# Kernel tuning notes

Hardware: AMD Instinct MI355X
Metric: run time of the kernel (lower is better)

## Reference

```python
import jax, jax.numpy as jnp
import numpy as np
import math

N = 60000; B = 2; D = 128; NH = 8; HD = D // NH; DFF = 256
NBLK = 6; L = NBLK * 2
WIN = 12.0; TEMP = 10000.0
NY, NX = 400, 400
MT = (36, 144)      # max_tokens per drop level (drop_info)
CAP = (25, 100)     # filled tokens per window in synthetic data (~0.7 fill)
LVL_N = (24000, 36000)  # voxels per drop level (per shift)


def _nwin(n, cap):
    return -(-n // cap)


def _make_inds(n, lvl):
    j = np.arange(n)
    return (j // CAP[lvl]) * MT[lvl] + (j % CAP[lvl])


def setup_inputs():
    ks = jax.random.split(jax.random.key(0), 8)
    rng = np.random.default_rng(0)
    # unique BEV coords per batch element -> scatter has no collisions
    coors_list = []
    for b in range(B):
        flat = rng.choice(NY * NX, N // B, replace=False)
        coors_list.append(np.stack([np.full(N // B, b, np.int64), np.zeros(N // B, np.int64), flat // NX, flat % NX], 1))
    coors = jnp.asarray(np.concatenate(coors_list, 0), dtype=jnp.int32)
    vxs, indss = [], []
    for s in range(2):
        perm = rng.permutation(N)
        vxs += [np.sort(perm[:LVL_N[0]]), np.sort(perm[LVL_N[0]:])]
        indss += [_make_inds(LVL_N[0], 0), _make_inds(LVL_N[1], 1)]
    i32 = lambda a: jnp.asarray(a, jnp.int32)
    f = lambda k, shape: jax.random.normal(k, shape, dtype=jnp.float32) * 0.02
    return dict(
        voxel_feat=jax.random.normal(ks[0], (N, D), dtype=jnp.float32),
        coors=coors,
        ciw0=jax.random.randint(ks[1], (N, 2), 0, int(WIN)).astype(jnp.float32),
        ciw1=jax.random.randint(ks[2], (N, 2), 0, int(WIN)).astype(jnp.float32),
        vx00=i32(vxs[0]), inds00=i32(indss[0]), vx01=i32(vxs[1]), inds01=i32(indss[1]),
        vx10=i32(vxs[2]), inds10=i32(indss[2]), vx11=i32(vxs[3]), inds11=i32(indss[3]),
        in_proj_w=f(ks[3], (L, 3 * D, D)), in_proj_b=jnp.zeros((L, 3 * D), jnp.float32),
        out_w=f(ks[4], (L, D, D)), out_b=jnp.zeros((L, D), jnp.float32),
        lin1_w=f(ks[5], (L, DFF, D)), lin1_b=jnp.zeros((L, DFF), jnp.float32),
        lin2_w=f(ks[6], (L, D, DFF)), lin2_b=jnp.zeros((L, D), jnp.float32),
        ln1_g=jnp.ones((L, D), jnp.float32), ln1_b=jnp.zeros((L, D), jnp.float32),
        ln2_g=jnp.ones((L, D), jnp.float32), ln2_b=jnp.zeros((L, D), jnp.float32),
        conv_w=f(ks[7], (2, D, D, 3, 3)),
        bn_g=jnp.ones((2, D), jnp.float32), bn_b=jnp.zeros((2, D), jnp.float32),
        bn_m=jnp.zeros((2, D), jnp.float32), bn_v=jnp.ones((2, D), jnp.float32),
    )


def _pos_embed(ciw):
    # SSTv1.get_pos_embed: interleaved sin/cos over x and y window coords
    xy = ciw - WIN / 2.0
    pl = D // 2
    i = jnp.arange(pl, dtype=jnp.float32)
    inv = TEMP ** (2.0 * jnp.floor(i / 2.0) / pl)
    e = xy[:, :, None] / inv                      # [N, 2, pl]
    emb = jnp.stack([jnp.sin(e[..., ::2]), jnp.cos(e[..., 1::2])], -1).reshape(ciw.shape[0], 2, pl)
    return jnp.concatenate([emb[:, 0], emb[:, 1]], -1)  # [N, D]


def _ln(x, g, b):
    mu = jnp.mean(x, -1, keepdims=True)
    var = jnp.mean((x - mu) ** 2, -1, keepdims=True)
    return (x - mu) * jax.lax.rsqrt(var + 1e-5) * g + b


def _forward(voxel_feat, coors, ciws, vx, inds, fp):
    (ipw, ipb, ow, ob, l1w, l1b, l2w, l2b, g1, b1, g2, b2, cw, bg, bb, bm, bv) = fp
    pos = [_pos_embed(ciws[0]), _pos_embed(ciws[1])]
    feat = voxel_feat
    for blk in range(NBLK):
        for s in range(2):  # BasicShiftBlock: one encoder layer per shift
            li = blk * 2 + s
            attn_out = jnp.zeros_like(feat)
            for lvl in range(2):  # drop levels, each with its own padded window tensor
                v, ii = vx[(s, lvl)], inds[(s, lvl)]
                mt = MT[lvl]
                nw = _nwin(int(v.shape[0]), CAP[lvl])
                def to_win(x2d):  # flat2window: scatter voxels into [nw, mt, C]
                    return jnp.zeros((nw * mt, x2d.shape[-1]), x2d.dtype).at[ii].set(x2d[v]).reshape(nw, mt, -1)
                wf = to_win(feat)
                wp = to_win(pos[s])
                pad = jnp.ones((nw * mt,), bool).at[ii].set(False).reshape(nw, mt)  # True = padded slot
                qk_in = wf + wp
                q = (qk_in @ ipw[li, :D].T + ipb[li, :D]).reshape(nw, mt, NH, HD)
                k = (qk_in @ ipw[li, D:2 * D].T + ipb[li, D:2 * D]).reshape(nw, mt, NH, HD)
                val = (wf @ ipw[li, 2 * D:].T + ipb[li, 2 * D:]).reshape(nw, mt, NH, HD)
                sc = jnp.einsum('wqhd,wkhd->whqk', q, k) / math.sqrt(HD)
                sc = jnp.where(pad[:, None, None, :], -jnp.inf, sc)
                o = jnp.einsum('whqk,wkhd->wqhd', jax.nn.softmax(sc, -1), val).reshape(nw, mt, D)
                o = o @ ow[li].T + ob[li]
                # window2flat: gather valid slots back to flat voxel order
                attn_out = attn_out.at[v].set(o.reshape(nw * mt, D)[ii])
            feat = _ln(feat + attn_out, g1[li], b1[li])
            h = jax.nn.gelu(feat @ l1w[li].T + l1b[li], approximate=False)
            feat = _ln(feat + h @ l2w[li].T + l2b[li], g2[li], b2[li])
    # recover_bev: scatter voxels into dense BEV canvas [B, C, ny, nx]
    flat_idx = coors[:, 0] * (NY * NX) + coors[:, 2] * NX + coors[:, 3]
    canvas = jnp.zeros((B * NY * NX, D), feat.dtype).at[flat_idx].set(feat)
    bev = canvas.reshape(B, NY, NX, D).transpose(0, 3, 1, 2)
    for i in range(2):  # attached dilated convs + BN(eval) + ReLU
        bev = jax.lax.conv_general_dilated(bev, cw[i], (1, 1), [(2, 2), (2, 2)], rhs_dilation=(2, 2), dimension_numbers=('NCHW', 'OIHW', 'NCHW'))
        bev = (bev - bm[i][:, None, None]) * jax.lax.rsqrt(bv[i][:, None, None] + 1e-3) * bg[i][:, None, None] + bb[i][:, None, None]
        bev = jax.nn.relu(bev)
    return bev


def reference(voxel_feat, coors, ciw0, ciw1, vx00, inds00, vx01, inds01, vx10, inds10, vx11, inds11, in_proj_w, in_proj_b, out_w, out_b, lin1_w, lin1_b, lin2_w, lin2_b, ln1_g, ln1_b, ln2_g, ln2_b, conv_w, bn_g, bn_b, bn_m, bn_v):
    vx = {(0, 0): vx00, (0, 1): vx01, (1, 0): vx10, (1, 1): vx11}
    inds = {(0, 0): inds00, (0, 1): inds01, (1, 0): inds10, (1, 1): inds11}
    fp = (in_proj_w, in_proj_b, out_w, out_b, lin1_w, lin1_b, lin2_w, lin2_b, ln1_g, ln1_b, ln2_g, ln2_b, conv_w, bn_g, bn_b, bn_m, bn_v)
    return _forward(voxel_feat, coors, (ciw0, ciw1), vx, inds, fp)
```

## Files before the change

kernel.cpp:

```cpp
#include <hip/hip_runtime.h>
#include <math.h>

#define NVOX 60000

typedef __attribute__((ext_vector_type(8))) short short8v;
typedef __attribute__((ext_vector_type(8))) unsigned short ushort8v;
typedef __attribute__((ext_vector_type(4))) float f32x4;

static __device__ __forceinline__ unsigned short f2bf(float f) {
    unsigned u = __float_as_uint(f);
    unsigned r = (u + 0x7fffu + ((u >> 16) & 1u)) >> 16;
    return (unsigned short)r;
}
static __device__ __forceinline__ float bf2f(unsigned short h) {
    return __uint_as_float(((unsigned)h) << 16);
}
static __device__ __forceinline__ void gll16(const unsigned short* g, unsigned short* l) {
    __builtin_amdgcn_global_load_lds(
        (const __attribute__((address_space(1))) unsigned*)g,
        (__attribute__((address_space(3))) unsigned*)l,
        16, 0, 0);
}

__global__ __launch_bounds__(256) void pos_kernel(const float* __restrict__ ciw,
                                                  unsigned short* __restrict__ pos) {
    int idx = blockIdx.x * 256 + threadIdx.x;
    if (idx >= NVOX * 128) return;
    int n = idx >> 7, d = idx & 127;
    int c = d >> 6, t = (d & 63) >> 1;
    float xy = ciw[n * 2 + c] - 6.0f;
    float inv = exp2f((float)t * (13.287712379549449f / 32.0f));
    float e = xy / inv;
    pos[idx] = f2bf((d & 1) ? cosf(e) : sinf(e));
}

__global__ __launch_bounds__(256) void cvt_bf16(const float* __restrict__ in,
                                                unsigned short* __restrict__ out, int n) {
    int idx = blockIdx.x * 256 + threadIdx.x;
    if (idx < n) out[idx] = f2bf(in[idx]);
}

__global__ __launch_bounds__(256) void feat_init(const float* __restrict__ vf,
                                                 float* __restrict__ feat,
                                                 unsigned short* __restrict__ featb) {
    int idx = blockIdx.x * 256 + threadIdx.x;
    if (idx >= NVOX * 128) return;
    float v = vf[idx];
    feat[idx] = v;
    featb[idx] = f2bf(v);
}

template<int KTOT, bool ADD, bool GELU, bool CBF16, bool LNF>
__global__ __launch_bounds__(256) void gemm_mfma(
    const unsigned short* __restrict__ A, const unsigned short* __restrict__ Aadd, int add_nblk,
    const unsigned short* __restrict__ W, const float* __restrict__ bias,
    void* __restrict__ Cp, int M, int ldc,
    float* __restrict__ feat, unsigned short* __restrict__ featb,
    const float* __restrict__ lng, const float* __restrict__ lnb)
{
    __shared__ unsigned short smem[128 * 128];
    __shared__ float2 lnsum[128][2];
    unsigned short* As = smem;
    unsigned short* Ws = smem + 128 * 64;
    const int tid = threadIdx.x;
    const int lane = tid & 63, wave = tid >> 6;
    const int wr = wave >> 1, wc = wave & 1;
    const int llo = lane & 15, lhi = lane >> 4;
    const int m0 = blockIdx.x * 128;
    const int n0 = blockIdx.y * 128;
    const bool addp = ADD && ((int)blockIdx.y < add_nblk);
    const int gr = lane >> 3;
    const int gc = (lane & 7) ^ gr;
    f32x4 acc[4][4] = {};

    for (int k0 = 0; k0 < KTOT; k0 += 64) {
        #pragma unroll
        for (int p = 0; p < 4; ++p) {
            int r0 = wave * 32 + p * 8;
            gll16(W + (size_t)(n0 + r0 + gr) * KTOT + k0 + gc * 8, &Ws[r0 * 64]);
        }
        if (!addp) {
            #pragma unroll
            for (int p = 0; p < 4; ++p) {
                int r0 = wave * 32 + p * 8;
                gll16(A + (size_t)(m0 + r0 + gr) * KTOT + k0 + gc * 8, &As[r0 * 64]);
            }
        } else {
            #pragma unroll
            for (int p = 0; p < 4; ++p) {
                int c = tid + p * 256;
                int r = c >> 3, c16 = c & 7;
                int m = m0 + r;
                short8v av = {};
                if (m < M) {
                    ushort8v fa = *reinterpret_cast<const ushort8v*>(A + (size_t)m * KTOT + k0 + c16 * 8);
                    ushort8v pa = *reinterpret_cast<const ushort8v*>(Aadd + (size_t)m * 128 + k0 + c16 * 8);
                    #pragma unroll
                    for (int q = 0; q < 8; ++q) av[q] = (short)f2bf(bf2f(fa[q]) + bf2f(pa[q]));
                }
                *reinterpret_cast<short8v*>((char*)As + r * 128 + ((c16 * 16) ^ ((r & 7) << 4))) = av;
            }
        }
        __syncthreads();
        #pragma unroll
        for (int kk = 0; kk < 2; ++kk) {
            int kb = kk * 64 + lhi * 16;
            short8v af[4], bf[4];
            #pragma unroll
            for (int i = 0; i < 4; ++i) {
                int r = wr * 64 + i * 16 + llo;
                af[i] = *reinterpret_cast<const short8v*>((const char*)As + r * 128 + (kb ^ ((r & 7) << 4)));
                int cc = wc * 64 + i * 16 + llo;
                bf[i] = *reinterpret_cast<const short8v*>((const char*)Ws + cc * 128 + (kb ^ ((cc & 7) << 4)));
            }
            #pragma unroll
            for (int i = 0; i < 4; ++i)
                #pragma unroll
                for (int j = 0; j < 4; ++j)
                    acc[i][j] = __builtin_amdgcn_mfma_f32_16x16x32_bf16(af[i], bf[j], acc[i][j], 0, 0, 0);
        }
        __syncthreads();
    }

    if (LNF) {
        float s1[4][4] = {}, s2[4][4] = {};
        #pragma unroll
        for (int i = 0; i < 4; ++i)
            #pragma unroll
            for (int rg = 0; rg < 4; ++rg) {
                int m = m0 + wr * 64 + i * 16 + lhi * 4 + rg;
                if (m < M) {
                    #pragma unroll
                    for (int j = 0; j < 4; ++j) {
                        int n = wc * 64 + j * 16 + llo;
                        float x = feat[(size_t)m * 128 + n] + acc[i][j][rg] + bias[n];
                        acc[i][j][rg] = x;
                        s1[i][rg] += x; s2[i][rg] += x * x;
                    }
                }
            }
        #pragma unroll
        for (int i = 0; i < 4; ++i)
            #pragma unroll
            for (int rg = 0; rg < 4; ++rg) {
                #pragma unroll
                for (int off = 1; off < 16; off <<= 1) {
                    s1[i][rg] += __shfl_xor(s1[i][rg], off);
                    s2[i][rg] += __shfl_xor(s2[i][rg], off);
                }
                if (llo == 0)
                    lnsum[wr * 64 + i * 16 + lhi * 4 + rg][wc] = make_float2(s1[i][rg], s2[i][rg]);
            }
        __syncthreads();
        #pragma unroll
        for (int i = 0; i < 4; ++i)
            #pragma unroll
            for (int rg = 0; rg < 4; ++rg) {
                int r = wr * 64 + i * 16 + lhi * 4 + rg;
                int m = m0 + r;
                if (m >= M) continue;
                float2 a0 = lnsum[r][0], a1 = lnsum[r][1];
                float mu = (a0.x + a1.x) * 0.0078125f;
                float var = fmaxf((a0.y + a1.y) * 0.0078125f - mu * mu, 0.f);
                float inv = rsqrtf(var + 1e-5f);
                #pragma unroll
                for (int j = 0; j < 4; ++j) {
                    int n = wc * 64 + j * 16 + llo;
                    float v = (acc[i][j][rg] - mu) * inv * lng[n] + lnb[n];
                    feat[(size_t)m * 128 + n] = v;
                    featb[(size_t)m * 128 + n] = f2bf(v);
                }
            }
    } else if (CBF16) {
        #pragma unroll
        for (int j = 0; j < 4; ++j) {
            int nl = wc * 64 + j * 16 + llo;
            float bn = bias[n0 + nl];
            #pragma unroll
            for (int i = 0; i < 4; ++i)
                #pragma unroll
                for (int rg = 0; rg < 4; ++rg) {
                    float v = acc[i][j][rg] + bn;
                    if (GELU) v = 0.5f * v * (1.0f + erff(v * 0.7071067811865475f));
                    smem[(wr * 64 + i * 16 + lhi * 4 + rg) * 128 + nl] = f2bf(v);
                }
        }
        __syncthreads();
        unsigned short* C = (unsigned short*)Cp;
        #pragma unroll
        for (int c = 0; c < 8; ++c) {
            int idx = tid + c * 256;
            int r = idx >> 4, ch = idx & 15;
            if (m0 + r < M)
                *reinterpret_cast<ushort8v*>(C + (size_t)(m0 + r) * ldc + n0 + ch * 8) =
                    *reinterpret_cast<const ushort8v*>(&smem[r * 128 + ch * 8]);
        }
    } else {
        float* C = (float*)Cp;
        #pragma unroll
        for (int j = 0; j < 4; ++j) {
            int n = n0 + wc * 64 + j * 16 + llo;
            float bn = bias[n];
            #pragma unroll
            for (int i = 0; i < 4; ++i)
                #pragma unroll
                for (int rg = 0; rg < 4; ++rg) {
                    int m = m0 + wr * 64 + i * 16 + lhi * 4 + rg;
                    if (m < M) {
                        float v = acc[i][j][rg] + bn;
                        if (GELU) v = 0.5f * v * (1.0f + erff(v * 0.7071067811865475f));
                        C[(size_t)m * ldc + n] = v;
                    }
                }
        }
    }
}

template<int CAPT, int HG>
__global__ __launch_bounds__(256) void attn_kernel(
    const unsigned short* __restrict__ qkv, const int* __restrict__ vlist, int nvox,
    unsigned short* __restrict__ oout)
{
    __shared__ float Ks[CAPT][HG * 16];
    __shared__ float Vs[CAPT][HG * 16];
    __shared__ int vl[CAPT];
    const int w = blockIdx.x;
    const int hb = blockIdx.y * HG;
    const int tid = threadIdx.x;
    const int T = min(CAPT, nvox - w * CAPT);
    if (tid < T) vl[tid] = vlist[w * CAPT + tid];
    constexpr int R8 = HG * 2;
    for (int idx = tid; idx < T * R8; idx += 256) {
        int t = idx / R8, c8 = (idx % R8) * 8;
        int vox = vlist[w * CAPT + t];
        const unsigned short* base = qkv + (size_t)vox * 384 + hb * 16 + c8;
        ushort8v kv = *reinterpret_cast<const ushort8v*>(base + 128);
        ushort8v vv = *reinterpret_cast<const ushort8v*>(base + 256);
        #pragma unroll
        for (int q = 0; q < 8; ++q) { Ks[t][c8 + q] = bf2f(kv[q]); Vs[t][c8 + q] = bf2f(vv[q]); }
    }
    __syncthreads();
    const int ITEMS = T * HG;
    for (int item = tid; item < ITEMS; item += 256) {
        int h = item & (HG - 1);
        int q = item / HG;
        int vq = vl[q];
        const unsigned short* qb = qkv + (size_t)vq * 384 + (hb + h) * 16;
        ushort8v qa = *reinterpret_cast<const ushort8v*>(qb);
        ushort8v qc = *reinterpret_cast<const ushort8v*>(qb + 8);
        float4 q0 = make_float4(bf2f(qa[0]), bf2f(qa[1]), bf2f(qa[2]), bf2f(qa[3]));
        float4 q1 = make_float4(bf2f(qa[4]), bf2f(qa[5]), bf2f(qa[6]), bf2f(qa[7]));
        float4 q2 = make_float4(bf2f(qc[0]), bf2f(qc[1]), bf2f(qc[2]), bf2f(qc[3]));
        float4 q3 = make_float4(bf2f(qc[4]), bf2f(qc[5]), bf2f(qc[6]), bf2f(qc[7]));
        float mx = -INFINITY, l = 0.f;
        float4 o0 = make_float4(0,0,0,0), o1 = o0, o2 = o0, o3 = o0;
        for (int t = 0; t < T; ++t) {
            const float4* kr = reinterpret_cast<const float4*>(&Ks[t][h * 16]);
            float4 k0 = kr[0], k1 = kr[1], k2 = kr[2], k3 = kr[3];
            float s = q0.x*k0.x + q0.y*k0.y + q0.z*k0.z + q0.w*k0.w
                    + q1.x*k1.x + q1.y*k1.y + q1.z*k1.z + q1.w*k1.w
                    + q2.x*k2.x + q2.y*k2.y + q2.z*k2.z + q2.w*k2.w
                    + q3.x*k3.x + q3.y*k3.y + q3.z*k3.z + q3.w*k3.w;
            s *= 0.25f;
            float mo = mx;
            mx = fmaxf(mx, s);
            float cc = __expf(mo - mx);
            float p  = __expf(s - mx);
            l = l * cc + p;
            const float4* vr = reinterpret_cast<const float4*>(&Vs[t][h * 16]);
            float4 v0 = vr[0], v1 = vr[1], v2 = vr[2], v3 = vr[3];
            o0.x = o0.x*cc + p*v0.x; o0.y = o0.y*cc + p*v0.y; o0.z = o0.z*cc + p*v0.z; o0.w = o0.w*cc + p*v0.w;
            o1.x = o1.x*cc + p*v1.x; o1.y = o1.y*cc + p*v1.y; o1.z = o1.z*cc + p*v1.z; o1.w = o1.w*cc + p*v1.w;
            o2.x = o2.x*cc + p*v2.x; o2.y = o2.y*cc + p*v2.y; o2.z = o2.z*cc + p*v2.z; o2.w = o2.w*cc + p*v2.w;
            o3.x = o3.x*cc + p*v3.x; o3.y = o3.y*cc + p*v3.y; o3.z = o3.z*cc + p*v3.z; o3.w = o3.w*cc + p*v3.w;
        }
        float rl = 1.0f / l;
        ushort8v r0, r1;
        r0[0]=f2bf(o0.x*rl); r0[1]=f2bf(o0.y*rl); r0[2]=f2bf(o0.z*rl); r0[3]=f2bf(o0.w*rl);
        r0[4]=f2bf(o1.x*rl); r0[5]=f2bf(o1.y*rl); r0[6]=f2bf(o1.z*rl); r0[7]=f2bf(o1.w*rl);
        r1[0]=f2bf(o2.x*rl); r1[1]=f2bf(o2.y*rl); r1[2]=f2bf(o2.z*rl); r1[3]=f2bf(o2.w*rl);
        r1[4]=f2bf(o3.x*rl); r1[5]=f2bf(o3.y*rl); r1[6]=f2bf(o3.z*rl); r1[7]=f2bf(o3.w*rl);
        unsigned short* op = oout + (size_t)vq * 128 + (hb + h) * 16;
        *reinterpret_cast<ushort8v*>(op) = r0;
        *reinterpret_cast<ushort8v*>(op + 8) = r1;
    }
}

__global__ __launch_bounds__(256) void scatter_kernel(const float* __restrict__ feat,
    const int* __restrict__ coors, unsigned short* __restrict__ canvas)
{
    int idx = blockIdx.x * 256 + threadIdx.x;
    if (idx >= NVOX * 16) return;
    int n = idx >> 4, c8 = (idx & 15) << 3;
    int b = coors[n * 4], y = coors[n * 4 + 2], x = coors[n * 4 + 3];
    const float* src = feat + (size_t)n * 128 + c8;
    float4 u0 = *reinterpret_cast<const float4*>(src);
    float4 u1 = *reinterpret_cast<const float4*>(src + 4);
    ushort8v v;
    v[0]=f2bf(u0.x); v[1]=f2bf(u0.y); v[2]=f2bf(u0.z); v[3]=f2bf(u0.w);
    v[4]=f2bf(u1.x); v[5]=f2bf(u1.y); v[6]=f2bf(u1.z); v[7]=f2bf(u1.w);
    size_t p = (((size_t)b * 404 + y + 2) * 420 + x + 2) * 128 + c8;
    *reinterpret_cast<ushort8v*>(canvas + p) = v;
}

__global__ __launch_bounds__(256) void halo_zero(unsigned short* __restrict__ c) {
    int idx = blockIdx.x * 256 + threadIdx.x;
    if (idx >= 2 * 9680 * 16) return;
    int b = idx / (9680 * 16);
    int rem = idx % (9680 * 16);
    int p = rem >> 4, ch = (rem & 15) * 8;
    int y, x;
    if (p < 1680) { int ry = p / 420; y = (ry < 2) ? ry : ry + 400; x = p % 420; }
    else { int q = p - 1680; y = 2 + q / 20; int cx = q % 20; x = (cx < 2) ? cx : cx + 400; }
    ushort8v z = {};
    *reinterpret_cast<ushort8v*>(c + (((size_t)b * 404 + y) * 420 + x) * 128 + ch) = z;
}

__global__ __launch_bounds__(256) void wtrans_kernel(const float* __restrict__ cw,
                                                     unsigned short* __restrict__ wbuf)
{
    int idx = blockIdx.x * 256 + threadIdx.x;
    if (idx >= 2 * 9 * 128 * 128) return;
    int ci = idx & 127;
    int co = (idx >> 7) & 127;
    int kk = (idx >> 14) % 9;
    int i  = idx / (9 * 16384);
    wbuf[idx] = f2bf(cw[(((size_t)i * 128 + co) * 128 + ci) * 9 + kk]);
}

template<bool NCHW_OUT>
__global__ __launch_bounds__(512, 1) void conv_mfma(
    const unsigned short* __restrict__ in, const unsigned short* __restrict__ wbuf,
    const float* __restrict__ g, const float* __restrict__ bsh,
    const float* __restrict__ bm, const float* __restrict__ bv,
    void* __restrict__ out)
{
    __shared__ unsigned short Ab[8 * 36 * 128];
    __shared__ unsigned short Wb[2 * 128 * 128];
    const int tid = threadIdx.x;
    const int lane = tid & 63, wave = tid >> 6;
    const int cog = wave & 1, yg = wave >> 1;
    const int llo = lane & 15, lhi = lane >> 4;
    const int x0 = blockIdx.x * 32, y0 = blockIdx.y * 4, b = blockIdx.z;
    const int c16s = lane & 15;

    #pragma unroll
    for (int it = 0; it < 9; ++it) {
        int gidx = it * 32 + wave * 4 + lhi;
        int row = gidx / 36, xi = gidx % 36;
        gll16(in + (((size_t)b * 404 + y0 + row) * 420 + x0 + xi) * 128 + ((c16s ^ (xi & 15)) * 8),
              Ab + (size_t)(it * 512 + wave * 64) * 8);
    }
    {
        const unsigned short* wt = wbuf;
        #pragma unroll
        for (int it = 0; it < 4; ++it) {
            int co = it * 32 + wave * 4 + lhi;
            gll16(wt + co * 128 + ((c16s ^ (co & 15)) * 8),
                  Wb + (size_t)(it * 512 + wave * 64) * 8);
        }
    }
    __syncthreads();

    f32x4 acc[2][4] = {};
    #pragma unroll
    for (int t = 0; t < 9; ++t) {
        if (t < 8) {
            const unsigned short* wt = wbuf + (size_t)(t + 1) * 16384;
            unsigned short* dst = Wb + ((t + 1) & 1) * 16384;
            #pragma unroll
            for (int it = 0; it < 4; ++it) {
                int co = it * 32 + wave * 4 + lhi;
                gll16(wt + co * 128 + ((c16s ^ (co & 15)) * 8),
                      dst + (size_t)(it * 512 + wave * 64) * 8);
            }
        }
        const unsigned short* Wp = Wb + (t & 1) * 16384;
        const int ky = t / 3, kx = t % 3;
        const int r = yg + 2 * ky;
        #pragma unroll
        for (int kk = 0; kk < 4; ++kk) {
            short8v a[2], w[4];
            #pragma unroll
            for (int i = 0; i < 2; ++i) {
                int xi = i * 16 + llo + 2 * kx;
                a[i] = *reinterpret_cast<const short8v*>(
                    (const char*)Ab + (r * 36 + xi) * 256 + ((kk * 64 + lhi * 16) ^ ((xi & 15) << 4)));
            }
            #pragma unroll
            for (int j = 0; j < 4; ++j) {
                int co = cog * 64 + j * 16 + llo;
                w[j] = *reinterpret_cast<const short8v*>(
                    (const char*)Wp + co * 256 + ((kk * 64 + lhi * 16) ^ ((co & 15) << 4)));
            }
            #pragma unroll
            for (int i = 0; i < 2; ++i)
                #pragma unroll
                for (int j = 0; j < 4; ++j)
                    acc[i][j] = __builtin_amdgcn_mfma_f32_16x16x32_bf16(a[i], w[j], acc[i][j], 0, 0, 0);
        }
        __syncthreads();
    }

    const int y = y0 + yg;
    if (NCHW_OUT) {
        #pragma unroll
        for (int j = 0; j < 4; ++j) {
            int co = cog * 64 + j * 16 + llo;
            float scale = rsqrtf(bv[co] + 1e-3f) * g[co];
            float shift = bsh[co] - bm[co] * scale;
            #pragma unroll
            for (int i = 0; i < 2; ++i) {
                int px = x0 + i * 16 + lhi * 4;
                if (px < 400) {
                    float4 v;
                    v.x = fmaxf(acc[i][j][0] * scale + shift, 0.f);
                    v.y = fmaxf(acc[i][j][1] * scale + shift, 0.f);
                    v.z = fmaxf(acc[i][j][2] * scale + shift, 0.f);
                    v.w = fmaxf(acc[i][j][3] * scale + shift, 0.f);
                    *reinterpret_cast<float4*>(
                        (float*)out + (((size_t)b * 128 + co) * 400 + y) * 400 + px) = v;
                }
            }
        }
    } else {
        unsigned short* Cw = Wb + wave * 2048;
        #pragma unroll
        for (int j = 0; j < 4; ++j) {
            int co = cog * 64 + j * 16 + llo;
            float scale = rsqrtf(bv[co] + 1e-3f) * g[co];
            float shift = bsh[co] - bm[co] * scale;
            #pragma unroll
            for (int i = 0; i < 2; ++i)
                #pragma unroll
                for (int rg = 0; rg < 4; ++rg)
                    Cw[(i * 16 + lhi * 4 + rg) * 64 + j * 16 + llo] =
                        f2bf(fmaxf(acc[i][j][rg] * scale + shift, 0.f));
        }
        #pragma unroll
        for (int s = 0; s < 4; ++s) {
            int pxl = s * 8 + (lane >> 3);
            int oct = lane & 7;
            int px = x0 + pxl;
            if (px < 400)
                *reinterpret_cast<ushort8v*>(
                    (unsigned short*)out + (((size_t)b * 404 + y + 2) * 420 + px + 2) * 128
                                         + cog * 64 + oct * 8) =
                    *reinterpret_cast<const ushort8v*>(&Cw[pxl * 64 + oct * 8]);
        }
    }
}

extern "C" void kernel_launch(void* const* d_in, const int* in_sizes, int n_in,
                              void* d_out, int out_size, void* d_ws, size_t ws_size,
                              hipStream_t stream) {
    const float* voxel_feat = (const float*)d_in[0];
    const int*   coors      = (const int*)d_in[1];
    const float* ciw0       = (const float*)d_in[2];
    const float* ciw1       = (const float*)d_in[3];
    const int* vx[2][2] = {{(const int*)d_in[4], (const int*)d_in[6]},
                           {(const int*)d_in[8], (const int*)d_in[10]}};
    const float* ipw = (const float*)d_in[12];
    const float* ipb = (const float*)d_in[13];
    const float* ow  = (const float*)d_in[14];
    const float* obp = (const float*)d_in[15];
    const float* l1w = (const float*)d_in[16];
    const float* l1b = (const float*)d_in[17];
    const float* l2w = (const float*)d_in[18];
    const float* l2b = (const float*)d_in[19];
    const float* g1  = (const float*)d_in[20];
    const float* b1  = (const float*)d_in[21];
    const float* g2  = (const float*)d_in[22];
    const float* b2  = (const float*)d_in[23];
    const float* cw  = (const float*)d_in[24];
    const float* bng = (const float*)d_in[25];
    const float* bnb = (const float*)d_in[26];
    const float* bnm = (const float*)d_in[27];
    const float* bnv = (const float*)d_in[28];

    float* F = (float*)d_ws;
    unsigned short* W0   = (unsigned short*)F;
    unsigned short* ipwb = W0;
    unsigned short* owb  = W0 + 589824;
    unsigned short* l1wb = W0 + 786432;
    unsigned short* l2wb = W0 + 1179648;
    unsigned short* cwb  = W0 + 1572864;
    float* feat = F + 940000;
    unsigned short* featb = (unsigned short*)(F + 8620000);
    unsigned short* pos0  = (unsigned short*)(F + 12460000);
    unsigned short* pos1  = (unsigned short*)(F + 16300000);
    unsigned short* obufb = (unsigned short*)(F + 20140000);
    unsigned short* hbufb = (unsigned short*)(F + 23980000);
    unsigned short* canvas1 = (unsigned short*)(F + 8620000);
    unsigned short* canvas2 = (unsigned short*)(F + 30339040);
    unsigned short* qkvb = (unsigned short*)d_out;

    feat_init<<<30000, 256, 0, stream>>>(voxel_feat, feat, featb);
    pos_kernel<<<30000, 256, 0, stream>>>(ciw0, pos0);
    pos_kernel<<<30000, 256, 0, stream>>>(ciw1, pos1);
    cvt_bf16<<<(589824 + 255) / 256, 256, 0, stream>>>(ipw, ipwb, 589824);
    cvt_bf16<<<(196608 + 255) / 256, 256, 0, stream>>>(ow,  owb,  196608);
    cvt_bf16<<<(393216 + 255) / 256, 256, 0, stream>>>(l1w, l1wb, 393216);
    cvt_bf16<<<(393216 + 255) / 256, 256, 0, stream>>>(l2w, l2wb, 393216);
    wtrans_kernel<<<(2 * 9 * 16384 + 255) / 256, 256, 0, stream>>>(cw, cwb);

    for (int li = 0; li < 12; ++li) {
        int s = li & 1;
        const unsigned short* pos = s ? pos1 : pos0;
        gemm_mfma<128, true, false, true, false><<<dim3(469, 3), 256, 0, stream>>>(
            featb, pos, 2, ipwb + (size_t)li * 49152, ipb + li * 384, qkvb, NVOX, 384,
            nullptr, nullptr, nullptr, nullptr);
        attn_kernel<25, 8><<<dim3(960, 1), 256, 0, stream>>>(qkvb, vx[s][0], 24000, obufb);
        attn_kernel<100, 2><<<dim3(360, 4), 256, 0, stream>>>(qkvb, vx[s][1], 36000, obufb);
        gemm_mfma<128, false, false, false, true><<<dim3(469, 1), 256, 0, stream>>>(
            obufb, nullptr, 0, owb + (size_t)li * 16384, obp + li * 128, nullptr, NVOX, 128,
            feat, featb, g1 + li * 128, b1 + li * 128);
        gemm_mfma<128, false, true, true, false><<<dim3(469, 2), 256, 0, stream>>>(
            featb, nullptr, 0, l1wb + (size_t)li * 32768, l1b + li * 256, hbufb, NVOX, 256,
            nullptr, nullptr, nullptr, nullptr);
        gemm_mfma<256, false, false, false, true><<<dim3(469, 1), 256, 0, stream>>>(
            hbufb, nullptr, 0, l2wb + (size_t)li * 32768, l2b + li * 128, nullptr, NVOX, 128,
            feat, featb, g2 + li * 128, b2 + li * 128);
    }

    hipMemsetAsync(canvas1, 0, (size_t)43438080 * 2, stream);
    halo_zero<<<(2 * 9680 * 16 + 255) / 256, 256, 0, stream>>>(canvas2);
    scatter_kernel<<<(NVOX * 16 + 255) / 256, 256, 0, stream>>>(feat, coors, canvas1);
    conv_mfma<false><<<dim3(13, 100, 2), 512, 0, stream>>>(
        canvas1, cwb, bng, bnb, bnm, bnv, canvas2);
    conv_mfma<true><<<dim3(13, 100, 2), 512, 0, stream>>>(
        canvas2, cwb + 9 * 16384, bng + 128, bnb + 128, bnm + 128, bnv + 128, (float*)d_out);
}
```

Measured before the change: 2.524 ms.

## Drop fp32 residual stream, keep bf16 features only, merge attention launches

Removes the fp32 copy of the residual features, so the LayerNorm epilogues read the residual from the bf16 buffer and write only bf16. The scatter kernel now copies bf16 features directly. The two attention kernels for the two drop levels are merged into one launch that picks its configuration from the block index. This cuts fp32 read/write traffic and one launch per layer, but the residual stream now accumulates in bf16 across 12 layers, which risks accuracy drift.

```diff
diff --git a/kernel.cpp b/kernel.cpp
--- a/kernel.cpp
+++ b/kernel.cpp
@@ -40,22 +40,12 @@
     if (idx < n) out[idx] = f2bf(in[idx]);
 }
 
-__global__ __launch_bounds__(256) void feat_init(const float* __restrict__ vf,
-                                                 float* __restrict__ feat,
-                                                 unsigned short* __restrict__ featb) {
-    int idx = blockIdx.x * 256 + threadIdx.x;
-    if (idx >= NVOX * 128) return;
-    float v = vf[idx];
-    feat[idx] = v;
-    featb[idx] = f2bf(v);
-}
-
 template<int KTOT, bool ADD, bool GELU, bool CBF16, bool LNF>
 __global__ __launch_bounds__(256) void gemm_mfma(
     const unsigned short* __restrict__ A, const unsigned short* __restrict__ Aadd, int add_nblk,
     const unsigned short* __restrict__ W, const float* __restrict__ bias,
     void* __restrict__ Cp, int M, int ldc,
-    float* __restrict__ feat, unsigned short* __restrict__ featb,
+    unsigned short* __restrict__ featb,
     const float* __restrict__ lng, const float* __restrict__ lnb)
 {
     __shared__ unsigned short smem[128 * 128];
@@ -133,7 +123,7 @@
                     #pragma unroll
                     for (int j = 0; j < 4; ++j) {
                         int n = wc * 64 + j * 16 + llo;
-                        float x = feat[(size_t)m * 128 + n] + acc[i][j][rg] + bias[n];
+                        float x = bf2f(featb[(size_t)m * 128 + n]) + acc[i][j][rg] + bias[n];
                         acc[i][j][rg] = x;
                         s1[i][rg] += x; s2[i][rg] += x * x;
                     }
@@ -167,7 +157,6 @@
                 for (int j = 0; j < 4; ++j) {
                     int n = wc * 64 + j * 16 + llo;
                     float v = (acc[i][j][rg] - mu) * inv * lng[n] + lnb[n];
-                    feat[(size_t)m * 128 + n] = v;
                     featb[(size_t)m * 128 + n] = f2bf(v);
                 }
             }
@@ -216,34 +205,40 @@
     }
 }
 
-template<int CAPT, int HG>
-__global__ __launch_bounds__(256) void attn_kernel(
-    const unsigned short* __restrict__ qkv, const int* __restrict__ vlist, int nvox,
-    unsigned short* __restrict__ oout)
+__global__ __launch_bounds__(256) void attn_merged(
+    const unsigned short* __restrict__ qkv, const int* __restrict__ vl0,
+    const int* __restrict__ vl1, unsigned short* __restrict__ oout)
 {
-    __shared__ float Ks[CAPT][HG * 16];
-    __shared__ float Vs[CAPT][HG * 16];
-    __shared__ int vl[CAPT];
-    const int w = blockIdx.x;
-    const int hb = blockIdx.y * HG;
+    __shared__ float Ks[3200];
+    __shared__ float Vs[3200];
+    __shared__ int vl[100];
+    int T, HGsh, hb, w;
+    const int* vlist;
+    if ((int)blockIdx.x < 960) {
+        T = 25; HGsh = 3; hb = 0; w = blockIdx.x; vlist = vl0;
+    } else {
+        int idx = blockIdx.x - 960;
+        T = 100; HGsh = 1; hb = (idx / 360) * 2; w = idx % 360; vlist = vl1;
+    }
+    const int HG = 1 << HGsh;
+    const int rs = HG * 16;
     const int tid = threadIdx.x;
-    const int T = min(CAPT, nvox - w * CAPT);
-    if (tid < T) vl[tid] = vlist[w * CAPT + tid];
-    constexpr int R8 = HG * 2;
-    for (int idx = tid; idx < T * R8; idx += 256) {
-        int t = idx / R8, c8 = (idx % R8) * 8;
-        int vox = vlist[w * CAPT + t];
+    if (tid < T) vl[tid] = vlist[w * T + tid];
+    const int r8sh = HGsh + 1;
+    for (int idx = tid; idx < (T << r8sh); idx += 256) {
+        int t = idx >> r8sh, c8 = (idx & ((1 << r8sh) - 1)) * 8;
+        int vox = vlist[w * T + t];
         const unsigned short* base = qkv + (size_t)vox * 384 + hb * 16 + c8;
         ushort8v kv = *reinterpret_cast<const ushort8v*>(base + 128);
         ushort8v vv = *reinterpret_cast<const ushort8v*>(base + 256);
         #pragma unroll
-        for (int q = 0; q < 8; ++q) { Ks[t][c8 + q] = bf2f(kv[q]); Vs[t][c8 + q] = bf2f(vv[q]); }
+        for (int q = 0; q < 8; ++q) { Ks[t * rs + c8 + q] = bf2f(kv[q]); Vs[t * rs + c8 + q] = bf2f(vv[q]); }
     }
     __syncthreads();
-    const int ITEMS = T * HG;
+    const int ITEMS = T << HGsh;
     for (int item = tid; item < ITEMS; item += 256) {
         int h = item & (HG - 1);
-        int q = item / HG;
+        int q = item >> HGsh;
         int vq = vl[q];
         const unsigned short* qb = qkv + (size_t)vq * 384 + (hb + h) * 16;
         ushort8v qa = *reinterpret_cast<const ushort8v*>(qb);
@@ -254,8 +249,10 @@
         float4 q3 = make_float4(bf2f(qc[4]), bf2f(qc[5]), bf2f(qc[6]), bf2f(qc[7]));
         float mx = -INFINITY, l = 0.f;
         float4 o0 = make_float4(0,0,0,0), o1 = o0, o2 = o0, o3 = o0;
+        const float* kbase = Ks + h * 16;
+        const float* vbase = Vs + h * 16;
         for (int t = 0; t < T; ++t) {
-            const float4* kr = reinterpret_cast<const float4*>(&Ks[t][h * 16]);
+            const float4* kr = reinterpret_cast<const float4*>(kbase + t * rs);
             float4 k0 = kr[0], k1 = kr[1], k2 = kr[2], k3 = kr[3];
             float s = q0.x*k0.x + q0.y*k0.y + q0.z*k0.z + q0.w*k0.w
                     + q1.x*k1.x + q1.y*k1.y + q1.z*k1.z + q1.w*k1.w
@@ -267,7 +264,7 @@
             float cc = __expf(mo - mx);
             float p  = __expf(s - mx);
             l = l * cc + p;
-            const float4* vr = reinterpret_cast<const float4*>(&Vs[t][h * 16]);
+            const float4* vr = reinterpret_cast<const float4*>(vbase + t * rs);
             float4 v0 = vr[0], v1 = vr[1], v2 = vr[2], v3 = vr[3];
             o0.x = o0.x*cc + p*v0.x; o0.y = o0.y*cc + p*v0.y; o0.z = o0.z*cc + p*v0.z; o0.w = o0.w*cc + p*v0.w;
             o1.x = o1.x*cc + p*v1.x; o1.y = o1.y*cc + p*v1.y; o1.z = o1.z*cc + p*v1.z; o1.w = o1.w*cc + p*v1.w;
@@ -286,21 +283,16 @@
     }
 }
 
-__global__ __launch_bounds__(256) void scatter_kernel(const float* __restrict__ feat,
+__global__ __launch_bounds__(256) void scatter_kernel(const unsigned short* __restrict__ featb,
     const int* __restrict__ coors, unsigned short* __restrict__ canvas)
 {
     int idx = blockIdx.x * 256 + threadIdx.x;
     if (idx >= NVOX * 16) return;
     int n = idx >> 4, c8 = (idx & 15) << 3;
     int b = coors[n * 4], y = coors[n * 4 + 2], x = coors[n * 4 + 3];
-    const float* src = feat + (size_t)n * 128 + c8;
-    float4 u0 = *reinterpret_cast<const float4*>(src);
-    float4 u1 = *reinterpret_cast<const float4*>(src + 4);
-    ushort8v v;
-    v[0]=f2bf(u0.x); v[1]=f2bf(u0.y); v[2]=f2bf(u0.z); v[3]=f2bf(u0.w);
-    v[4]=f2bf(u1.x); v[5]=f2bf(u1.y); v[6]=f2bf(u1.z); v[7]=f2bf(u1.w);
     size_t p = (((size_t)b * 404 + y + 2) * 420 + x + 2) * 128 + c8;
-    *reinterpret_cast<ushort8v*>(canvas + p) = v;
+    *reinterpret_cast<ushort8v*>(canvas + p) =
+        *reinterpret_cast<const ushort8v*>(featb + (size_t)n * 128 + c8);
 }
 
 __global__ __launch_bounds__(256) void halo_zero(unsigned short* __restrict__ c) {
@@ -485,17 +477,16 @@
     unsigned short* l1wb = W0 + 786432;
     unsigned short* l2wb = W0 + 1179648;
     unsigned short* cwb  = W0 + 1572864;
-    float* feat = F + 940000;
-    unsigned short* featb = (unsigned short*)(F + 8620000);
-    unsigned short* pos0  = (unsigned short*)(F + 12460000);
-    unsigned short* pos1  = (unsigned short*)(F + 16300000);
-    unsigned short* obufb = (unsigned short*)(F + 20140000);
-    unsigned short* hbufb = (unsigned short*)(F + 23980000);
+    unsigned short* featb = (unsigned short*)(F + 940000);
+    unsigned short* pos0  = (unsigned short*)(F + 4780000);
+    unsigned short* pos1  = (unsigned short*)(F + 8620000);
+    unsigned short* obufb = (unsigned short*)(F + 12460000);
+    unsigned short* hbufb = (unsigned short*)(F + 16300000);
     unsigned short* canvas1 = (unsigned short*)(F + 8620000);
     unsigned short* canvas2 = (unsigned short*)(F + 30339040);
     unsigned short* qkvb = (unsigned short*)d_out;
 
-    feat_init<<<30000, 256, 0, stream>>>(voxel_feat, feat, featb);
+    cvt_bf16<<<30000, 256, 0, stream>>>(voxel_feat, featb, NVOX * 128);
     pos_kernel<<<30000, 256, 0, stream>>>(ciw0, pos0);
     pos_kernel<<<30000, 256, 0, stream>>>(ciw1, pos1);
     cvt_bf16<<<(589824 + 255) / 256, 256, 0, stream>>>(ipw, ipwb, 589824);
@@ -509,23 +500,22 @@
         const unsigned short* pos = s ? pos1 : pos0;
         gemm_mfma<128, true, false, true, false><<<dim3(469, 3), 256, 0, stream>>>(
             featb, pos, 2, ipwb + (size_t)li * 49152, ipb + li * 384, qkvb, NVOX, 384,
-            nullptr, nullptr, nullptr, nullptr);
-        attn_kernel<25, 8><<<dim3(960, 1), 256, 0, stream>>>(qkvb, vx[s][0], 24000, obufb);
-        attn_kernel<100, 2><<<dim3(360, 4), 256, 0, stream>>>(qkvb, vx[s][1], 36000, obufb);
+            nullptr, nullptr, nullptr);
+        attn_merged<<<2400, 256, 0, stream>>>(qkvb, vx[s][0], vx[s][1], obufb);
         gemm_mfma<128, false, false, false, true><<<dim3(469, 1), 256, 0, stream>>>(
             obufb, nullptr, 0, owb + (size_t)li * 16384, obp + li * 128, nullptr, NVOX, 128,
-            feat, featb, g1 + li * 128, b1 + li * 128);
+            featb, g1 + li * 128, b1 + li * 128);
         gemm_mfma<128, false, true, true, false><<<dim3(469, 2), 256, 0, stream>>>(
             featb, nullptr, 0, l1wb + (size_t)li * 32768, l1b + li * 256, hbufb, NVOX, 256,
-            nullptr, nullptr, nullptr, nullptr);
+            nullptr, nullptr, nullptr);
         gemm_mfma<256, false, false, false, true><<<dim3(469, 1), 256, 0, stream>>>(
             hbufb, nullptr, 0, l2wb + (size_t)li * 32768, l2b + li * 128, nullptr, NVOX, 128,
-            feat, featb, g2 + li * 128, b2 + li * 128);
+            featb, g2 + li * 128, b2 + li * 128);
     }
 
     hipMemsetAsync(canvas1, 0, (size_t)43438080 * 2, stream);
     halo_zero<<<(2 * 9680 * 16 + 255) / 256, 256, 0, stream>>>(canvas2);
-    scatter_kernel<<<(NVOX * 16 + 255) / 256, 256, 0, stream>>>(feat, coors, canvas1);
+    scatter_kernel<<<(NVOX * 16 + 255) / 256, 256, 0, stream>>>(featb, coors, canvas1);
     conv_mfma<false><<<dim3(13, 100, 2), 512, 0, stream>>>(
         canvas1, cwb, bng, bnb, bnm, bnv, canvas2);
     conv_mfma<true><<<dim3(13, 100, 2), 512, 0, stream>>>(
```

Result: faster. 2.340 ms (-7.3%).
